# Kernel tuning notes

Hardware: AMD Instinct MI355X
Metric: run time of the kernel (lower is better)

Reference implementation:

```python
import jax, jax.numpy as jnp
import numpy as np

N_NODES = 50000
N_EDGES = 800000
F_IN = 32
H = 128
LN_EPS = 1e-5


def _gcn_layer(h, src, tgt, w_self, b_self, w_neigh, b_neigh):
    # h: [N, D]; src/tgt: [E]
    n = h.shape[0]
    self_feat = h @ w_self + b_self                      # [N, Dout]
    src_feat = h[src]                                    # [E, D] gather
    agg = jax.ops.segment_sum(src_feat, tgt, num_segments=n)          # [N, D]
    cnt = jax.ops.segment_sum(jnp.ones((src.shape[0],), h.dtype), tgt,
                              num_segments=n)[:, None]   # [N, 1]
    agg = agg / jnp.maximum(cnt, 1.0)
    return self_feat + agg @ w_neigh + b_neigh


def _layer_norm(x, gamma, beta):
    mu = jnp.mean(x, axis=-1, keepdims=True)
    var = jnp.mean(jnp.square(x - mu), axis=-1, keepdims=True)
    return (x - mu) * jax.lax.rsqrt(var + LN_EPS) * gamma + beta


def setup_inputs() -> dict:
    key = jax.random.key(0)
    ks = jax.random.split(key, 16)
    s_in = 1.0 / np.sqrt(F_IN)
    s_h = 1.0 / np.sqrt(H)
    inp = {
        "x": jax.random.normal(ks[0], (N_NODES, F_IN), jnp.float32),
        "edge_index": jax.random.randint(ks[1], (2, N_EDGES), 0, N_NODES, jnp.int64)
        if jax.config.jax_enable_x64 else
        jax.random.randint(ks[1], (2, N_EDGES), 0, N_NODES, jnp.int32),
        "w_in": jax.random.uniform(ks[2], (F_IN, H), jnp.float32, -s_in, s_in),
        "b_in": jax.random.uniform(ks[3], (H,), jnp.float32, -s_in, s_in),
        "ws0": jax.random.uniform(ks[4], (H, H), jnp.float32, -s_h, s_h),
        "bs0": jax.random.uniform(ks[5], (H,), jnp.float32, -s_h, s_h),
        "wn0": jax.random.uniform(ks[6], (H, H), jnp.float32, -s_h, s_h),
        "bn0": jax.random.uniform(ks[7], (H,), jnp.float32, -s_h, s_h),
        "g0": jnp.ones((H,), jnp.float32),
        "be0": jnp.zeros((H,), jnp.float32),
        "ws1": jax.random.uniform(ks[8], (H, H), jnp.float32, -s_h, s_h),
        "bs1": jax.random.uniform(ks[9], (H,), jnp.float32, -s_h, s_h),
        "wn1": jax.random.uniform(ks[10], (H, H), jnp.float32, -s_h, s_h),
        "bn1": jax.random.uniform(ks[11], (H,), jnp.float32, -s_h, s_h),
        "g1": jnp.ones((H,), jnp.float32),
        "be1": jnp.zeros((H,), jnp.float32),
    }
    return inp


def reference(x, edge_index, w_in, b_in, ws0, bs0, wn0, bn0, g0, be0,
              ws1, bs1, wn1, bn1, g1, be1):
    src, tgt = edge_index[0], edge_index[1]
    h = jax.nn.relu(x @ w_in + b_in)                     # input_proj + relu
    # layer 0 (intermediate): gcn -> LN -> relu -> dropout(eval=id) -> residual
    residual = h
    h = _gcn_layer(h, src, tgt, ws0, bs0, wn0, bn0)
    h = _layer_norm(h, g0, be0)
    h = jax.nn.relu(h) + residual
    # layer 1 (final): gcn -> LN
    h = _gcn_layer(h, src, tgt, ws1, bs1, wn1, bn1)
    h = _layer_norm(h, g1, be1)
    return h
```

## Files before the change

### kernel.cpp

```cpp
#include <hip/hip_runtime.h>

#define H 128
#define CAP 64
typedef unsigned short ushort_t;
typedef __bf16 bf16x8 __attribute__((ext_vector_type(8)));
typedef unsigned short u16x8 __attribute__((ext_vector_type(8)));
typedef float f32x4 __attribute__((ext_vector_type(4)));
typedef float f32x2 __attribute__((ext_vector_type(2)));

__device__ __forceinline__ float bf2f(ushort_t b) {
    return __uint_as_float(((unsigned int)b) << 16);
}
__device__ __forceinline__ ushort_t f2bf(float f) {
    unsigned int u = __float_as_uint(f);
    unsigned int r = (u + 0x7fffu + ((u >> 16) & 1u)) >> 16;
    return (ushort_t)r;
}
__device__ __forceinline__ unsigned char f2fp8(float f) {
    int r = __builtin_amdgcn_cvt_pk_fp8_f32(f, f, 0, false);
    return (unsigned char)(r & 0xff);
}

__device__ __forceinline__
void pack_one(int idx, const float* __restrict__ W0, const float* __restrict__ W1,
              const float* __restrict__ b0, const float* __restrict__ b1,
              ushort_t* __restrict__ Wpack, float* __restrict__ bsum,
              int Ksplit, int K)
{
    int total = K * 16;
    if (idx < total) {
        int l = idx & 63, tt = (idx >> 6) & 7, s = idx >> 9;
        int c = tt * 16 + (l & 15);
        int kb = s * 32 + ((l >> 4) & 3) * 8;
#pragma unroll
        for (int j = 0; j < 8; ++j) {
            int k = kb + j;
            float v = (k < Ksplit) ? W0[(size_t)k * H + c]
                                   : W1[(size_t)(k - Ksplit) * H + c];
            Wpack[(size_t)idx * 8 + j] = f2bf(v);
        }
    }
    if (idx < H) bsum[idx] = b0[idx] + (b1 ? b1[idx] : 0.f);
}

__global__ __launch_bounds__(256)
void k_prep(const float* __restrict__ w_in, const float* __restrict__ b_in,
            const float* __restrict__ ws0, const float* __restrict__ bs0,
            const float* __restrict__ wn0, const float* __restrict__ bn0,
            const float* __restrict__ ws1, const float* __restrict__ bs1,
            const float* __restrict__ wn1, const float* __restrict__ bn1,
            ushort_t* __restrict__ Wpin, float* __restrict__ bin,
            ushort_t* __restrict__ Wp0, float* __restrict__ bsm0,
            ushort_t* __restrict__ Wp1, float* __restrict__ bsm1,
            int* __restrict__ fl, int N)
{
    int b = blockIdx.x, t = threadIdx.x;
    if (b < 2) {
        pack_one(b * 256 + t, w_in, w_in, b_in, nullptr, Wpin, bin, 32, 32);
    } else if (b < 18) {
        pack_one((b - 2) * 256 + t, ws0, wn0, bs0, bn0, Wp0, bsm0, 128, 256);
    } else if (b < 34) {
        pack_one((b - 18) * 256 + t, ws1, wn1, bs1, bn1, Wp1, bsm1, 128, 256);
    } else {
        int i = (b - 34) * 256 + t;
        if (i < N) fl[i] = 0;
    }
}

#define FILL_CHUNK 4096

template<int K, int DO_LN, int RESREL, int RELU, int OUTBF, int HQ, int AF32, int FILL>
__global__ __launch_bounds__(256)
void k_gemm_ln(const ushort_t* __restrict__ A, const float* __restrict__ Af, int lda,
               const ushort_t* __restrict__ Wpack,
               const float* __restrict__ bias,
               const float* __restrict__ g, const float* __restrict__ be,
               const ushort_t* __restrict__ resid, int ldr,
               float* __restrict__ Cf, ushort_t* __restrict__ Cb,
               unsigned char* __restrict__ hq, int ldc,
               const int* __restrict__ srcs, const int* __restrict__ tgts,
               int* __restrict__ fl, ushort_t* __restrict__ col, int E,
               int fillBlocks, int M)
{
    if (FILL) {
        if ((int)blockIdx.x < fillBlocks) {
            int b = blockIdx.x;
            int range = b & 7;
            int chunk = b >> 3;
            int lim = chunk * FILL_CHUNK + FILL_CHUNK;
            if (lim > E) lim = E;
            for (int i = chunk * FILL_CHUNK + threadIdx.x; i < lim; i += 256) {
                int tt = tgts[i];
                if ((tt >> 13) == range) {
                    int p = atomicAdd(&fl[tt], 1);
                    if (p < CAP) col[tt * CAP + p] = (ushort_t)srcs[i];
                }
            }
            return;
        }
    }
    const int bidm = FILL ? ((int)blockIdx.x - fillBlocks) : (int)blockIdx.x;

    constexpr int NS = K / 32;
    __shared__ ushort_t Bs[NS * 8 * 64 * 8];
    const int t = threadIdx.x;
    {
        const uint4* wsrc = (const uint4*)Wpack;
        uint4* wdst = (uint4*)Bs;
        constexpr int CH = K * 16;
#pragma unroll
        for (int i = t; i < CH; i += 256) wdst[i] = wsrc[i];
    }
    __syncthreads();

    const int wave = t >> 6, lane = t & 63;
    const int quad = lane >> 4, l16 = lane & 15;
    const int m0 = bidm * 128 + wave * 32;

    f32x4 acc[2][8];
#pragma unroll
    for (int mt = 0; mt < 2; ++mt)
#pragma unroll
        for (int nt = 0; nt < 8; ++nt) acc[mt][nt] = (f32x4){0.f, 0.f, 0.f, 0.f};

    bf16x8 afrag[NS][2];
#pragma unroll
    for (int s = 0; s < NS; ++s)
#pragma unroll
        for (int mt = 0; mt < 2; ++mt) {
            int row = m0 + mt * 16 + l16;
            if (row >= M) row = M - 1;
            if (AF32) {
                const float* p = Af + (size_t)row * lda + s * 32 + quad * 8;
                float4 v0 = *(const float4*)p;
                float4 v1 = *(const float4*)(p + 4);
                union { u16x8 u; bf16x8 b; } cv;
                cv.u[0] = f2bf(v0.x); cv.u[1] = f2bf(v0.y);
                cv.u[2] = f2bf(v0.z); cv.u[3] = f2bf(v0.w);
                cv.u[4] = f2bf(v1.x); cv.u[5] = f2bf(v1.y);
                cv.u[6] = f2bf(v1.z); cv.u[7] = f2bf(v1.w);
                afrag[s][mt] = cv.b;
            } else {
                afrag[s][mt] = *(const bf16x8*)(A + (size_t)row * lda + s * 32 + quad * 8);
            }
        }

    const bf16x8* bfr = (const bf16x8*)Bs;
#pragma unroll
    for (int s = 0; s < NS; ++s)
#pragma unroll
        for (int nt = 0; nt < 8; ++nt) {
            bf16x8 b = bfr[(s * 8 + nt) * 64 + lane];
#pragma unroll
            for (int mt = 0; mt < 2; ++mt)
                acc[mt][nt] = __builtin_amdgcn_mfma_f32_16x16x32_bf16(
                    afrag[s][mt], b, acc[mt][nt], 0, 0, 0);
        }

    float bv[8], gv[8], bev[8];
#pragma unroll
    for (int nt = 0; nt < 8; ++nt) {
        int c = nt * 16 + l16;
        bv[nt] = bias[c];
        if (DO_LN) { gv[nt] = g[c]; bev[nt] = be[c]; }
    }

#pragma unroll
    for (int mt = 0; mt < 2; ++mt)
#pragma unroll
        for (int r = 0; r < 4; ++r) {
            int row = m0 + mt * 16 + quad * 4 + r;
            float v[8];
#pragma unroll
            for (int nt = 0; nt < 8; ++nt) v[nt] = acc[mt][nt][r] + bv[nt];
            if (DO_LN) {
                float s1 = 0.f, s2 = 0.f;
#pragma unroll
                for (int nt = 0; nt < 8; ++nt) { s1 += v[nt]; s2 += v[nt] * v[nt]; }
#pragma unroll
                for (int mk = 1; mk < 16; mk <<= 1) {
                    s1 += __shfl_xor(s1, mk);
                    s2 += __shfl_xor(s2, mk);
                }
                float mu = s1 * (1.f / H);
                float var = s2 * (1.f / H) - mu * mu;
                float rs = rsqrtf(var + 1e-5f);
#pragma unroll
                for (int nt = 0; nt < 8; ++nt)
                    v[nt] = (v[nt] - mu) * rs * gv[nt] + bev[nt];
            }
            if (row < M) {
#pragma unroll
                for (int nt = 0; nt < 8; ++nt) {
                    int c = nt * 16 + l16;
                    float y = v[nt];
                    if (RELU) y = fmaxf(y, 0.f);
                    if (RESREL)
                        y = fmaxf(y, 0.f) + bf2f(resid[(size_t)row * ldr + c]);
                    if (OUTBF) Cb[(size_t)row * ldc + c] = f2bf(y);
                    else       Cf[(size_t)row * ldc + c] = y;
                    if (HQ) hq[(size_t)row * H + c] = f2fp8(y);
                }
            }
        }
}

__global__ __launch_bounds__(256)
void k_agg(const unsigned char* __restrict__ hq, const int* __restrict__ fl,
           const ushort_t* __restrict__ col, ushort_t* __restrict__ out, int n)
{
    int node = blockIdx.x * 4 + (threadIdx.x >> 6);
    if (node >= n) return;
    int lane = threadIdx.x & 63;
    int grp = lane >> 4, li = lane & 15;
    int cnt = fl[node];
    int m = cnt < CAP ? cnt : CAP;
    int beg = node * CAP, end = beg + m;
    float s[8];
#pragma unroll
    for (int j = 0; j < 8; ++j) s[j] = 0.f;

    int e = beg;
    for (; e + 16 <= end; e += 16) {
        uint2 v[4];
#pragma unroll
        for (int q = 0; q < 4; ++q) {
            int r = col[e + 4 * q + grp];
            v[q] = *(const uint2*)(hq + (size_t)r * 128 + li * 8);
        }
#pragma unroll
        for (int q = 0; q < 4; ++q) {
            f32x2 a0 = __builtin_amdgcn_cvt_pk_f32_fp8(v[q].x, false);
            f32x2 a1 = __builtin_amdgcn_cvt_pk_f32_fp8(v[q].x, true);
            f32x2 a2 = __builtin_amdgcn_cvt_pk_f32_fp8(v[q].y, false);
            f32x2 a3 = __builtin_amdgcn_cvt_pk_f32_fp8(v[q].y, true);
            s[0] += a0.x; s[1] += a0.y; s[2] += a1.x; s[3] += a1.y;
            s[4] += a2.x; s[5] += a2.y; s[6] += a3.x; s[7] += a3.y;
        }
    }
    if (e + 8 <= end) {
        uint2 v[2];
#pragma unroll
        for (int q = 0; q < 2; ++q) {
            int r = col[e + 4 * q + grp];
            v[q] = *(const uint2*)(hq + (size_t)r * 128 + li * 8);
        }
#pragma unroll
        for (int q = 0; q < 2; ++q) {
            f32x2 a0 = __builtin_amdgcn_cvt_pk_f32_fp8(v[q].x, false);
            f32x2 a1 = __builtin_amdgcn_cvt_pk_f32_fp8(v[q].x, true);
            f32x2 a2 = __builtin_amdgcn_cvt_pk_f32_fp8(v[q].y, false);
            f32x2 a3 = __builtin_amdgcn_cvt_pk_f32_fp8(v[q].y, true);
            s[0] += a0.x; s[1] += a0.y; s[2] += a1.x; s[3] += a1.y;
            s[4] += a2.x; s[5] += a2.y; s[6] += a3.x; s[7] += a3.y;
        }
        e += 8;
    }
    if (e + 4 <= end) {
        int r = col[e + grp];
        uint2 v0 = *(const uint2*)(hq + (size_t)r * 128 + li * 8);
        f32x2 a0 = __builtin_amdgcn_cvt_pk_f32_fp8(v0.x, false);
        f32x2 a1 = __builtin_amdgcn_cvt_pk_f32_fp8(v0.x, true);
        f32x2 a2 = __builtin_amdgcn_cvt_pk_f32_fp8(v0.y, false);
        f32x2 a3 = __builtin_amdgcn_cvt_pk_f32_fp8(v0.y, true);
        s[0] += a0.x; s[1] += a0.y; s[2] += a1.x; s[3] += a1.y;
        s[4] += a2.x; s[5] += a2.y; s[6] += a3.x; s[7] += a3.y;
        e += 4;
    }
    for (; e < end; ++e) {
        if (grp == 0) {
            int r = col[e];
            uint2 v0 = *(const uint2*)(hq + (size_t)r * 128 + li * 8);
            f32x2 a0 = __builtin_amdgcn_cvt_pk_f32_fp8(v0.x, false);
            f32x2 a1 = __builtin_amdgcn_cvt_pk_f32_fp8(v0.x, true);
            f32x2 a2 = __builtin_amdgcn_cvt_pk_f32_fp8(v0.y, false);
            f32x2 a3 = __builtin_amdgcn_cvt_pk_f32_fp8(v0.y, true);
            s[0] += a0.x; s[1] += a0.y; s[2] += a1.x; s[3] += a1.y;
            s[4] += a2.x; s[5] += a2.y; s[6] += a3.x; s[7] += a3.y;
        }
    }
#pragma unroll
    for (int j = 0; j < 8; ++j) {
        s[j] += __shfl_xor(s[j], 16);
        s[j] += __shfl_xor(s[j], 32);
    }
    if (grp == 0) {
        float inv = 1.f / fmaxf((float)cnt, 1.f);
        uint4 o;
        o.x = ((unsigned)f2bf(s[1] * inv) << 16) | f2bf(s[0] * inv);
        o.y = ((unsigned)f2bf(s[3] * inv) << 16) | f2bf(s[2] * inv);
        o.z = ((unsigned)f2bf(s[5] * inv) << 16) | f2bf(s[4] * inv);
        o.w = ((unsigned)f2bf(s[7] * inv) << 16) | f2bf(s[6] * inv);
        *(uint4*)(out + (size_t)node * 256 + li * 8) = o;
    }
}

extern "C" void kernel_launch(void* const* d_in, const int* in_sizes, int n_in,
                              void* d_out, int out_size, void* d_ws, size_t ws_size,
                              hipStream_t stream)
{
    const float* x    = (const float*)d_in[0];
    const int*   ei   = (const int*)d_in[1];
    const float* w_in = (const float*)d_in[2];
    const float* b_in = (const float*)d_in[3];
    const float* ws0  = (const float*)d_in[4];
    const float* bs0  = (const float*)d_in[5];
    const float* wn0  = (const float*)d_in[6];
    const float* bn0  = (const float*)d_in[7];
    const float* g0   = (const float*)d_in[8];
    const float* be0  = (const float*)d_in[9];
    const float* ws1  = (const float*)d_in[10];
    const float* bs1  = (const float*)d_in[11];
    const float* wn1  = (const float*)d_in[12];
    const float* bn1  = (const float*)d_in[13];
    const float* g1   = (const float*)d_in[14];
    const float* be1  = (const float*)d_in[15];

    const int N = in_sizes[0] / 32;
    const int E = in_sizes[1] / 2;
    const int* srcs = ei;
    const int* tgts = ei + E;

    char* w = (char*)d_ws;
    ushort_t* Acat0 = (ushort_t*)w;  w += (size_t)N * 256 * 2;
    ushort_t* Acat1 = (ushort_t*)w;  w += (size_t)N * 256 * 2;
    unsigned char* hq0 = (unsigned char*)w;  w += (size_t)N * H;
    unsigned char* hq1 = (unsigned char*)w;  w += (size_t)N * H;
    ushort_t* Wpin  = (ushort_t*)w;  w += 32 * H * 2;
    ushort_t* Wp0   = (ushort_t*)w;  w += 256 * H * 2;
    ushort_t* Wp1   = (ushort_t*)w;  w += 256 * H * 2;
    float* bin  = (float*)w;         w += H * 4;
    float* bsm0 = (float*)w;         w += H * 4;
    float* bsm1 = (float*)w;         w += H * 4;
    int* fl     = (int*)w;           w += (size_t)N * 4;
    ushort_t* col = (ushort_t*)w;    w += (size_t)N * CAP * 2;

    int gN = (N + 255) / 256;
    int gM = (N + 127) / 128;
    int gF = 8 * ((E + FILL_CHUNK - 1) / FILL_CHUNK);

    k_prep<<<34 + gN, 256, 0, stream>>>(
        w_in, b_in, ws0, bs0, wn0, bn0, ws1, bs1, wn1, bn1,
        Wpin, bin, Wp0, bsm0, Wp1, bsm1, fl, N);

    k_gemm_ln<32, 0, 0, 1, 1, 1, 1, 1><<<gF + gM, 256, 0, stream>>>(
        nullptr, x, 32, Wpin, bin, nullptr, nullptr, nullptr, 0,
        nullptr, Acat0, hq0, 256,
        srcs, tgts, fl, col, E, gF, N);

    k_agg<<<(N + 3) / 4, 256, 0, stream>>>(hq0, fl, col, Acat0 + 128, N);
    k_gemm_ln<256, 1, 1, 0, 1, 1, 0, 0><<<gM, 256, 0, stream>>>(
        Acat0, nullptr, 256, Wp0, bsm0, g0, be0, Acat0, 256,
        nullptr, Acat1, hq1, 256,
        nullptr, nullptr, nullptr, nullptr, 0, 0, N);

    k_agg<<<(N + 3) / 4, 256, 0, stream>>>(hq1, fl, col, Acat1 + 128, N);
    k_gemm_ln<256, 1, 0, 0, 0, 0, 0, 0><<<gM, 256, 0, stream>>>(
        Acat1, nullptr, 256, Wp1, bsm1, g1, be1, nullptr, 0,
        (float*)d_out, nullptr, nullptr, H,
        nullptr, nullptr, nullptr, nullptr, 0, 0, N);
}
```

Measured before the change: 224.3 us.

## Fuse neighbor aggregation into GEMM+LN kernels, dropping separate agg pass

Removes the standalone k_agg kernel and performs the fp8 neighbor gather-mean inside each layer's GEMM kernel. Each lane gathers neighbor rows directly into the MFMA A-fragment layout for the K=128..255 half. This avoids writing and re-reading the aggregated bf16 half of Acat and removes two launches, and the Acat buffers shrink to width H. In exchange, the gather now runs with one row per 16-lane group and wave-uniform max-degree loops. That gives less memory-level parallelism, divergence on low-degree rows, and serialized latency before the second half of the MFMAs.

```diff
diff --git a/kernel.cpp b/kernel.cpp
--- a/kernel.cpp
+++ b/kernel.cpp
@@ -19,6 +19,14 @@
 __device__ __forceinline__ unsigned char f2fp8(float f) {
     int r = __builtin_amdgcn_cvt_pk_fp8_f32(f, f, 0, false);
     return (unsigned char)(r & 0xff);
+}
+__device__ __forceinline__ void acc8(float* s, uint2 v) {
+    f32x2 a0 = __builtin_amdgcn_cvt_pk_f32_fp8(v.x, false);
+    f32x2 a1 = __builtin_amdgcn_cvt_pk_f32_fp8(v.x, true);
+    f32x2 a2 = __builtin_amdgcn_cvt_pk_f32_fp8(v.y, false);
+    f32x2 a3 = __builtin_amdgcn_cvt_pk_f32_fp8(v.y, true);
+    s[0] += a0.x; s[1] += a0.y; s[2] += a1.x; s[3] += a1.y;
+    s[4] += a2.x; s[5] += a2.y; s[6] += a3.x; s[7] += a3.y;
 }
 
 __device__ __forceinline__
@@ -69,7 +77,8 @@
 
 #define FILL_CHUNK 4096
 
-template<int K, int DO_LN, int RESREL, int RELU, int OUTBF, int HQ, int AF32, int FILL>
+template<int K, int DO_LN, int RESREL, int RELU, int OUTBF, int HQ,
+         int AF32, int FILL, int AGG>
 __global__ __launch_bounds__(256)
 void k_gemm_ln(const ushort_t* __restrict__ A, const float* __restrict__ Af, int lda,
                const ushort_t* __restrict__ Wpack,
@@ -78,6 +87,7 @@
                const ushort_t* __restrict__ resid, int ldr,
                float* __restrict__ Cf, ushort_t* __restrict__ Cb,
                unsigned char* __restrict__ hq, int ldc,
+               const unsigned char* __restrict__ hq_in,
                const int* __restrict__ srcs, const int* __restrict__ tgts,
                int* __restrict__ fl, ushort_t* __restrict__ col, int E,
                int fillBlocks, int M)
@@ -123,9 +133,10 @@
 #pragma unroll
         for (int nt = 0; nt < 8; ++nt) acc[mt][nt] = (f32x4){0.f, 0.f, 0.f, 0.f};
 
+    constexpr int NSH = AGG ? 4 : NS;
     bf16x8 afrag[NS][2];
 #pragma unroll
-    for (int s = 0; s < NS; ++s)
+    for (int s = 0; s < NSH; ++s)
 #pragma unroll
         for (int mt = 0; mt < 2; ++mt) {
             int row = m0 + mt * 16 + l16;
@@ -146,16 +157,89 @@
         }
 
     const bf16x8* bfr = (const bf16x8*)Bs;
-#pragma unroll
-    for (int s = 0; s < NS; ++s)
-#pragma unroll
-        for (int nt = 0; nt < 8; ++nt) {
-            bf16x8 b = bfr[(s * 8 + nt) * 64 + lane];
-#pragma unroll
-            for (int mt = 0; mt < 2; ++mt)
-                acc[mt][nt] = __builtin_amdgcn_mfma_f32_16x16x32_bf16(
-                    afrag[s][mt], b, acc[mt][nt], 0, 0, 0);
-        }
+
+    if (AGG) {
+#pragma unroll
+        for (int s = 0; s < 4; ++s)
+#pragma unroll
+            for (int nt = 0; nt < 8; ++nt) {
+                bf16x8 b = bfr[(s * 8 + nt) * 64 + lane];
+#pragma unroll
+                for (int mt = 0; mt < 2; ++mt)
+                    acc[mt][nt] = __builtin_amdgcn_mfma_f32_16x16x32_bf16(
+                        afrag[s][mt], b, acc[mt][nt], 0, 0, 0);
+            }
+
+#pragma unroll
+        for (int mt = 0; mt < 2; ++mt) {
+            int row = m0 + mt * 16 + l16;
+            if (row >= M) row = M - 1;
+            int cnt = fl[row];
+            int m = cnt < CAP ? cnt : CAP;
+            int mm = m;
+#pragma unroll
+            for (int mk = 1; mk < 64; mk <<= 1) {
+                int o = __shfl_xor(mm, mk);
+                mm = mm > o ? mm : o;
+            }
+            float sacc[4][8];
+#pragma unroll
+            for (int si = 0; si < 4; ++si)
+#pragma unroll
+                for (int j = 0; j < 8; ++j) sacc[si][j] = 0.f;
+
+            const ushort_t* cl = col + row * CAP;
+            for (int e = 0; e < mm; e += 2) {
+                uint2 v[2][4] = {{{0,0},{0,0},{0,0},{0,0}},
+                                 {{0,0},{0,0},{0,0},{0,0}}};
+#pragma unroll
+                for (int u = 0; u < 2; ++u) {
+                    if (e + u < m) {
+                        int rs = cl[e + u];
+                        const unsigned char* p = hq_in + (size_t)rs * 128 + quad * 8;
+                        v[u][0] = *(const uint2*)(p);
+                        v[u][1] = *(const uint2*)(p + 32);
+                        v[u][2] = *(const uint2*)(p + 64);
+                        v[u][3] = *(const uint2*)(p + 96);
+                    }
+                }
+#pragma unroll
+                for (int u = 0; u < 2; ++u)
+#pragma unroll
+                    for (int si = 0; si < 4; ++si) acc8(sacc[si], v[u][si]);
+            }
+            float inv = 1.f / fmaxf((float)cnt, 1.f);
+#pragma unroll
+            for (int si = 0; si < 4; ++si) {
+                union { u16x8 u; bf16x8 b; } cv;
+#pragma unroll
+                for (int j = 0; j < 8; ++j) cv.u[j] = f2bf(sacc[si][j] * inv);
+                afrag[4 + si][mt] = cv.b;
+            }
+        }
+
+#pragma unroll
+        for (int s = 4; s < 8; ++s)
+#pragma unroll
+            for (int nt = 0; nt < 8; ++nt) {
+                bf16x8 b = bfr[(s * 8 + nt) * 64 + lane];
+#pragma unroll
+                for (int mt = 0; mt < 2; ++mt)
+                    acc[mt][nt] = __builtin_amdgcn_mfma_f32_16x16x32_bf16(
+                        afrag[s][mt], b, acc[mt][nt], 0, 0, 0);
+            }
+    } else {
+#pragma unroll
+        for (int s = 0; s < NS; ++s)
+#pragma unroll
+            for (int nt = 0; nt < 8; ++nt) {
+                bf16x8 b = bfr[(s * 8 + nt) * 64 + lane];
+#pragma unroll
+                for (int mt = 0; mt < 2; ++mt)
+                    acc[mt][nt] = __builtin_amdgcn_mfma_f32_16x16x32_bf16(
+                        afrag[s][mt], b, acc[mt][nt], 0, 0, 0);
+            }
+    }
 
     float bv[8], gv[8], bev[8];
 #pragma unroll
@@ -203,96 +287,6 @@
                 }
             }
         }
-}
-
-__global__ __launch_bounds__(256)
-void k_agg(const unsigned char* __restrict__ hq, const int* __restrict__ fl,
-           const ushort_t* __restrict__ col, ushort_t* __restrict__ out, int n)
-{
-    int node = blockIdx.x * 4 + (threadIdx.x >> 6);
-    if (node >= n) return;
-    int lane = threadIdx.x & 63;
-    int grp = lane >> 4, li = lane & 15;
-    int cnt = fl[node];
-    int m = cnt < CAP ? cnt : CAP;
-    int beg = node * CAP, end = beg + m;
-    float s[8];
-#pragma unroll
-    for (int j = 0; j < 8; ++j) s[j] = 0.f;
-
-    int e = beg;
-    for (; e + 16 <= end; e += 16) {
-        uint2 v[4];
-#pragma unroll
-        for (int q = 0; q < 4; ++q) {
-            int r = col[e + 4 * q + grp];
-            v[q] = *(const uint2*)(hq + (size_t)r * 128 + li * 8);
-        }
-#pragma unroll
-        for (int q = 0; q < 4; ++q) {
-            f32x2 a0 = __builtin_amdgcn_cvt_pk_f32_fp8(v[q].x, false);
-            f32x2 a1 = __builtin_amdgcn_cvt_pk_f32_fp8(v[q].x, true);
-            f32x2 a2 = __builtin_amdgcn_cvt_pk_f32_fp8(v[q].y, false);
-            f32x2 a3 = __builtin_amdgcn_cvt_pk_f32_fp8(v[q].y, true);
-            s[0] += a0.x; s[1] += a0.y; s[2] += a1.x; s[3] += a1.y;
-            s[4] += a2.x; s[5] += a2.y; s[6] += a3.x; s[7] += a3.y;
-        }
-    }
-    if (e + 8 <= end) {
-        uint2 v[2];
-#pragma unroll
-        for (int q = 0; q < 2; ++q) {
-            int r = col[e + 4 * q + grp];
-            v[q] = *(const uint2*)(hq + (size_t)r * 128 + li * 8);
-        }
-#pragma unroll
-        for (int q = 0; q < 2; ++q) {
-            f32x2 a0 = __builtin_amdgcn_cvt_pk_f32_fp8(v[q].x, false);
-            f32x2 a1 = __builtin_amdgcn_cvt_pk_f32_fp8(v[q].x, true);
-            f32x2 a2 = __builtin_amdgcn_cvt_pk_f32_fp8(v[q].y, false);
-            f32x2 a3 = __builtin_amdgcn_cvt_pk_f32_fp8(v[q].y, true);
-            s[0] += a0.x; s[1] += a0.y; s[2] += a1.x; s[3] += a1.y;
-            s[4] += a2.x; s[5] += a2.y; s[6] += a3.x; s[7] += a3.y;
-        }
-        e += 8;
-    }
-    if (e + 4 <= end) {
-        int r = col[e + grp];
-        uint2 v0 = *(const uint2*)(hq + (size_t)r * 128 + li * 8);
-        f32x2 a0 = __builtin_amdgcn_cvt_pk_f32_fp8(v0.x, false);
-        f32x2 a1 = __builtin_amdgcn_cvt_pk_f32_fp8(v0.x, true);
-        f32x2 a2 = __builtin_amdgcn_cvt_pk_f32_fp8(v0.y, false);
-        f32x2 a3 = __builtin_amdgcn_cvt_pk_f32_fp8(v0.y, true);
-        s[0] += a0.x; s[1] += a0.y; s[2] += a1.x; s[3] += a1.y;
-        s[4] += a2.x; s[5] += a2.y; s[6] += a3.x; s[7] += a3.y;
-        e += 4;
-    }
-    for (; e < end; ++e) {
-        if (grp == 0) {
-            int r = col[e];
-            uint2 v0 = *(const uint2*)(hq + (size_t)r * 128 + li * 8);
-            f32x2 a0 = __builtin_amdgcn_cvt_pk_f32_fp8(v0.x, false);
-            f32x2 a1 = __builtin_amdgcn_cvt_pk_f32_fp8(v0.x, true);
-            f32x2 a2 = __builtin_amdgcn_cvt_pk_f32_fp8(v0.y, false);
-            f32x2 a3 = __builtin_amdgcn_cvt_pk_f32_fp8(v0.y, true);
-            s[0] += a0.x; s[1] += a0.y; s[2] += a1.x; s[3] += a1.y;
-            s[4] += a2.x; s[5] += a2.y; s[6] += a3.x; s[7] += a3.y;
-        }
-    }
-#pragma unroll
-    for (int j = 0; j < 8; ++j) {
-        s[j] += __shfl_xor(s[j], 16);
-        s[j] += __shfl_xor(s[j], 32);
-    }
-    if (grp == 0) {
-        float inv = 1.f / fmaxf((float)cnt, 1.f);
-        uint4 o;
-        o.x = ((unsigned)f2bf(s[1] * inv) << 16) | f2bf(s[0] * inv);
-        o.y = ((unsigned)f2bf(s[3] * inv) << 16) | f2bf(s[2] * inv);
-        o.z = ((unsigned)f2bf(s[5] * inv) << 16) | f2bf(s[4] * inv);
-        o.w = ((unsigned)f2bf(s[7] * inv) << 16) | f2bf(s[6] * inv);
-        *(uint4*)(out + (size_t)node * 256 + li * 8) = o;
-    }
 }
 
 extern "C" void kernel_launch(void* const* d_in, const int* in_sizes, int n_in,
@@ -322,8 +316,8 @@
     const int* tgts = ei + E;
 
     char* w = (char*)d_ws;
-    ushort_t* Acat0 = (ushort_t*)w;  w += (size_t)N * 256 * 2;
-    ushort_t* Acat1 = (ushort_t*)w;  w += (size_t)N * 256 * 2;
+    ushort_t* Acat0 = (ushort_t*)w;  w += (size_t)N * H * 2;
+    ushort_t* Acat1 = (ushort_t*)w;  w += (size_t)N * H * 2;
     unsigned char* hq0 = (unsigned char*)w;  w += (size_t)N * H;
     unsigned char* hq1 = (unsigned char*)w;  w += (size_t)N * H;
     ushort_t* Wpin  = (ushort_t*)w;  w += 32 * H * 2;
@@ -343,20 +337,18 @@
         w_in, b_in, ws0, bs0, wn0, bn0, ws1, bs1, wn1, bn1,
         Wpin, bin, Wp0, bsm0, Wp1, bsm1, fl, N);
 
-    k_gemm_ln<32, 0, 0, 1, 1, 1, 1, 1><<<gF + gM, 256, 0, stream>>>(
+    k_gemm_ln<32, 0, 0, 1, 1, 1, 1, 1, 0><<<gF + gM, 256, 0, stream>>>(
         nullptr, x, 32, Wpin, bin, nullptr, nullptr, nullptr, 0,
-        nullptr, Acat0, hq0, 256,
+        nullptr, Acat0, hq0, 128, nullptr,
         srcs, tgts, fl, col, E, gF, N);
 
-    k_agg<<<(N + 3) / 4, 256, 0, stream>>>(hq0, fl, col, Acat0 + 128, N);
-    k_gemm_ln<256, 1, 1, 0, 1, 1, 0, 0><<<gM, 256, 0, stream>>>(
-        Acat0, nullptr, 256, Wp0, bsm0, g0, be0, Acat0, 256,
-        nullptr, Acat1, hq1, 256,
-        nullptr, nullptr, nullptr, nullptr, 0, 0, N);
-
-    k_agg<<<(N + 3) / 4, 256, 0, stream>>>(hq1, fl, col, Acat1 + 128, N);
-    k_gemm_ln<256, 1, 0, 0, 0, 0, 0, 0><<<gM, 256, 0, stream>>>(
-        Acat1, nullptr, 256, Wp1, bsm1, g1, be1, nullptr, 0,
-        (float*)d_out, nullptr, nullptr, H,
-        nullptr, nullptr, nullptr, nullptr, 0, 0, N);
-}
+    k_gemm_ln<256, 1, 1, 0, 1, 1, 0, 0, 1><<<gM, 256, 0, stream>>>(
+        Acat0, nullptr, 128, Wp0, bsm0, g0, be0, Acat0, 128,
+        nullptr, Acat1, hq1, 128, hq0,
+        nullptr, nullptr, fl, col, 0, 0, N);
+
+    k_gemm_ln<256, 1, 0, 0, 0, 0, 0, 0, 1><<<gM, 256, 0, stream>>>(
+        Acat1, nullptr, 128, Wp1, bsm1, g1, be1, nullptr, 0,
+        (float*)d_out, nullptr, nullptr, H, hq1,
+        nullptr, nullptr, fl, col, 0, 0, N);
+}
```

Result: slower. 258.3 us (+15.2%).
